# Kernel tuning notes

Hardware: AMD Instinct MI355X
Metric: run time of the kernel (lower is better)

## Reference

```python
import jax, jax.numpy as jnp
import numpy as np

INF = 1000.0
T = 1.0
NQ, NS, D, C = 4096, 8192, 512, 1024


def setup_inputs() -> dict:
    key = jax.random.key(0)
    k1, k2, k3 = jax.random.split(key, 3)
    xq = jax.random.normal(k1, (NQ, D), dtype=jnp.float32)
    xs = jax.random.normal(k2, (NS, D), dtype=jnp.float32)
    yq = jax.random.randint(k3, (NQ,), 0, C, dtype=jnp.int32)
    # supports laid out so class c occupies indices c, c+C, c+2C, ...
    ys = (jnp.arange(NS) % C).astype(jnp.int32)
    # positive index for query i: first support of class yq[i] -> index yq[i]
    pos = yq.astype(jnp.int32)
    return {"xq": xq, "yq": yq, "xs": xs, "ys": ys, "pos": pos}


def reference(xq, yq, xs, ys, pos):
    nq = xq.shape[0]
    ind = jnp.arange(nq)

    # per-class support counts (classes are 0..C-1, all present)
    counts = jax.ops.segment_sum(jnp.ones_like(ys, dtype=jnp.float32), ys,
                                 num_segments=C)  # [C]

    class_mask = yq[:, None] == ys[None, :]            # [Nq, Ns]
    idx = jnp.sum(class_mask, axis=-1) > 1             # [Nq] class has >1 support
    # drop the positive from the mask where the class has other supports
    class_mask = class_mask.at[ind, pos].set(~idx)

    # l2 logit: -||xq - xs||^2 / 2 / T
    sq = (jnp.sum(xq * xq, axis=-1)[:, None]
          + jnp.sum(xs * xs, axis=-1)[None, :]
          - 2.0 * (xq @ xs.T))                          # [Nq, Ns]
    logit = -0.5 * sq / T

    # logit[ind,pos] *= 0 then -= INF where idx  ->  0 or -INF at the positive
    logit = logit.at[ind, pos].set(jnp.where(idx, -INF, 0.0))

    # per-class masked segment sum over supports: [Nq, C]
    summed = jax.ops.segment_sum(logit.T, ys, num_segments=C).T

    # counts with the query's own class decremented by 1
    adjusted_counts = counts[None, :] - jax.nn.one_hot(yq, C, dtype=jnp.float32)
    normalized = summed / adjusted_counts               # [Nq, C]

    neg_logit = jax.nn.logsumexp(normalized, axis=1, keepdims=True)  # [Nq,1]

    mask_f = class_mask.astype(logit.dtype)
    pos_logit = (jnp.sum(logit * mask_f, axis=-1)
                 / jnp.sum(mask_f, axis=-1))[:, None]   # [Nq,1]

    return jnp.mean(neg_logit - pos_logit)
```

## Files before the change

kernel.cpp:

```cpp
#include <hip/hip_runtime.h>

#define NQ 4096
#define NS 8192
#define DD 512
#define CC 1024
#define KSUP 8
#define TM 128
#define TN 128
#define TK 64
#define KTILES (DD / TK)
#define PARTS (CC / TN)
#define NPANEL (NQ / TM)
#define CBLK (CC / 4)
#define FP_SCALE 1099511627776.0

typedef __attribute__((ext_vector_type(4))) float f32x4;

__device__ __forceinline__ unsigned int pk4_fp8(float4 v) {
    int lo = __builtin_amdgcn_cvt_pk_fp8_f32(v.x, v.y, 0, false);
    int hi = __builtin_amdgcn_cvt_pk_fp8_f32(v.z, v.w, lo, true);
    return (unsigned int)hi;
}

__device__ __forceinline__ float wave_reduce(float v) {
    #pragma unroll
    for (int d = 32; d > 0; d >>= 1) v += __shfl_xor(v, d);
    return v;
}

__global__ __launch_bounds__(256) void prep_kernel(
    const float* __restrict__ xs, const float* __restrict__ xq,
    const int* __restrict__ pos,
    unsigned char* __restrict__ Sb, float* __restrict__ SN,
    unsigned char* __restrict__ xqb, float* __restrict__ qn,
    float* __restrict__ tpl, unsigned long long* __restrict__ acc_fixed,
    unsigned int* __restrict__ panel_cnt) {
    int b = blockIdx.x, t = threadIdx.x;
    int w = t >> 6, lane = t & 63;
    if (b < CBLK) {
        if (b == 0) {
            if (t < 2) acc_fixed[t] = 0ULL;
            if (t < NPANEL) panel_cnt[t] = 0u;
        }
        int c = 4 * b + w;
        float4 s0 = {0.f, 0.f, 0.f, 0.f}, s1 = {0.f, 0.f, 0.f, 0.f};
        float nrm = 0.f;
        #pragma unroll
        for (int k = 0; k < KSUP; ++k) {
            const float4* rowp = (const float4*)(xs + (size_t)(c + k * CC) * DD);
            float4 v0 = rowp[lane];
            float4 v1 = rowp[lane + 64];
            s0.x += v0.x; s0.y += v0.y; s0.z += v0.z; s0.w += v0.w;
            s1.x += v1.x; s1.y += v1.y; s1.z += v1.z; s1.w += v1.w;
            nrm += v0.x * v0.x + v0.y * v0.y + v0.z * v0.z + v0.w * v0.w
                 + v1.x * v1.x + v1.y * v1.y + v1.z * v1.z + v1.w * v1.w;
        }
        unsigned int* dst = (unsigned int*)(Sb + (size_t)c * DD);
        dst[lane]      = pk4_fp8(s0);
        dst[lane + 64] = pk4_fp8(s1);
        nrm = wave_reduce(nrm);
        if (lane == 0) SN[c] = nrm;
    } else {
        int half = t >> 7, tt = t & 127;
        __shared__ float ws0[4], ws1[4], ws2[4];
        int i = 2 * (b - CBLK) + half;
        int j = pos[i];
        float4 q = ((const float4*)(xq + (size_t)i * DD))[tt];
        float4 s = ((const float4*)(xs + (size_t)j * DD))[tt];
        ((unsigned int*)(xqb + (size_t)i * DD))[tt] = pk4_fp8(q);
        float a  = q.x * q.x + q.y * q.y + q.z * q.z + q.w * q.w;
        float bd = q.x * s.x + q.y * s.y + q.z * s.z + q.w * s.w;
        float c2 = s.x * s.x + s.y * s.y + s.z * s.z + s.w * s.w;
        a = wave_reduce(a); bd = wave_reduce(bd); c2 = wave_reduce(c2);
        if (lane == 0) { ws0[w] = a; ws1[w] = bd; ws2[w] = c2; }
        __syncthreads();
        if (tt == 0) {
            float A  = ws0[2 * half] + ws0[2 * half + 1];
            float B  = ws1[2 * half] + ws1[2 * half + 1];
            float C2 = ws2[2 * half] + ws2[2 * half + 1];
            qn[i] = A;
            tpl[i] = -0.5f * (A + C2) + B;
        }
    }
}

__global__ __launch_bounds__(512, 2) void gemm_fused_kernel(
    const unsigned char* __restrict__ Abf,
    const unsigned char* __restrict__ Bbf,
    const float* __restrict__ SN, const float* __restrict__ qn,
    const float* __restrict__ tpl, const int* __restrict__ yq,
    float2* __restrict__ partials,
    float* __restrict__ pos_out,
    unsigned int* __restrict__ panel_cnt,
    unsigned long long* __restrict__ acc_fixed, float* __restrict__ out) {
    __shared__ __align__(16) char smem[131072];
    __shared__ unsigned int last_flag;
    __shared__ float red2[8];
    char* As = smem;
    char* Bs = smem + 65536;

    int lin = blockIdx.y * PARTS + blockIdx.x;
    int xcd = lin & 7;
    int k_in = lin >> 3;
    int bm = 4 * xcd + (k_in >> 3);
    int bn = k_in & 7;

    int t = threadIdx.x;
    int lane = t & 63, w = t >> 6;
    int wr = w & 1, wc = w >> 1;
    int r16 = lane & 15, halfk = lane >> 4;

    const int rowA0 = bm * TM;
    const int rowB0 = bn * TN;

    #pragma unroll
    for (int u = 0; u < 8; ++u) {
        int p = t + u * 512;
        int row = p >> 5, s16 = p & 31;
        int src16 = s16 ^ (row & 15);
        __builtin_amdgcn_global_load_lds(
            (const __attribute__((address_space(1))) unsigned int*)(Abf + (size_t)(rowA0 + row) * DD + src16 * 16),
            (__attribute__((address_space(3))) unsigned int*)(As + p * 16), 16, 0, 0);
    }
    #pragma unroll
    for (int u = 0; u < 8; ++u) {
        int p = t + u * 512;
        int row = p >> 5, s16 = p & 31;
        int src16 = s16 ^ (row & 15);
        __builtin_amdgcn_global_load_lds(
            (const __attribute__((address_space(1))) unsigned int*)(Bbf + (size_t)(rowB0 + row) * DD + src16 * 16),
            (__attribute__((address_space(3))) unsigned int*)(Bs + p * 16), 16, 0, 0);
    }
    asm volatile("s_waitcnt vmcnt(0)" ::: "memory");
    __builtin_amdgcn_s_barrier();
    asm volatile("" ::: "memory");

    f32x4 acc[4][2] = {};
    #pragma unroll
    for (int kt = 0; kt < KTILES; ++kt) {
        long a[4][2], bb[2][2];
        #pragma unroll
        for (int mi = 0; mi < 4; ++mi)
            #pragma unroll
            for (int kk = 0; kk < 2; ++kk) {
                int row = wr * 64 + mi * 16 + r16;
                int hk8 = kt * 8 + kk * 4 + halfk;
                a[mi][kk] = *(const long*)(As + row * 512 + ((hk8 ^ ((row & 15) << 1)) << 3));
            }
        #pragma unroll
        for (int ni = 0; ni < 2; ++ni)
            #pragma unroll
            for (int kk = 0; kk < 2; ++kk) {
                int row = wc * 32 + ni * 16 + r16;
                int hk8 = kt * 8 + kk * 4 + halfk;
                bb[ni][kk] = *(const long*)(Bs + row * 512 + ((hk8 ^ ((row & 15) << 1)) << 3));
            }
        #pragma unroll
        for (int kk = 0; kk < 2; ++kk)
            #pragma unroll
            for (int mi = 0; mi < 4; ++mi)
                #pragma unroll
                for (int ni = 0; ni < 2; ++ni)
                    acc[mi][ni] = __builtin_amdgcn_mfma_f32_16x16x32_fp8_fp8(a[mi][kk], bb[ni][kk], acc[mi][ni], 0, 0, 0);
    }

    __syncthreads();

    float* e_qn  = (float*)smem;
    float* e_tpl = e_qn + TM;
    int*   e_y   = (int*)(e_tpl + TM);
    float* e_sn  = (float*)(e_y + TM);
    float* e_max = e_sn + TN;
    float* e_sum = e_max + TM * 4;

    if (t < TM) {
        e_qn[t]  = qn[rowA0 + t];
        e_tpl[t] = tpl[rowA0 + t];
        e_y[t]   = yq[rowA0 + t];
    }
    if (t < TN) e_sn[t] = SN[rowB0 + t];
    __syncthreads();

    #pragma unroll
    for (int mi = 0; mi < 4; ++mi) {
        #pragma unroll
        for (int r = 0; r < 4; ++r) {
            int row_l = wr * 64 + mi * 16 + halfk * 4 + r;
            float base = -4.0f * e_qn[row_l];
            int yv = e_y[row_l];
            float v[2];
            #pragma unroll
            for (int ni = 0; ni < 2; ++ni) {
                int col_l = wc * 32 + ni * 16 + r16;
                float s = acc[mi][ni][r] + base - 0.5f * e_sn[col_l];
                if (rowB0 + col_l == yv) {
                    s = s - e_tpl[row_l] - 1000.0f;
                    v[ni] = s * (1.0f / 7.0f);
                    pos_out[rowA0 + row_l] = (s + 1000.0f) * (1.0f / 7.0f);
                } else {
                    v[ni] = s * 0.125f;
                }
            }
            float m = fmaxf(v[0], v[1]);
            #pragma unroll
            for (int d = 1; d < 16; d <<= 1) m = fmaxf(m, __shfl_xor(m, d));
            float sm = __expf(v[0] - m) + __expf(v[1] - m);
            #pragma unroll
            for (int d = 1; d < 16; d <<= 1) sm += __shfl_xor(sm, d);
            if (r16 == 0) {
                e_max[row_l * 4 + wc] = m;
                e_sum[row_l * 4 + wc] = sm;
            }
        }
    }
    __syncthreads();
    if (t < TM) {
        float m0 = e_max[t * 4], m1 = e_max[t * 4 + 1];
        float m2 = e_max[t * 4 + 2], m3 = e_max[t * 4 + 3];
        float g = fmaxf(fmaxf(m0, m1), fmaxf(m2, m3));
        float gs = e_sum[t * 4]     * __expf(m0 - g)
                 + e_sum[t * 4 + 1] * __expf(m1 - g)
                 + e_sum[t * 4 + 2] * __expf(m2 - g)
                 + e_sum[t * 4 + 3] * __expf(m3 - g);
        partials[(size_t)(rowA0 + t) * PARTS + bn] = make_float2(g, gs);
    }
    __syncthreads();

    if (t == 0) {
        unsigned int old = atomicAdd(&panel_cnt[bm], 1u);
        last_flag = (old == PARTS - 1) ? 1u : 0u;
    }
    __syncthreads();
    asm volatile("" ::: "memory");
    if (last_flag) {
        float loss = 0.f;
        if (t < TM) {
            int row = rowA0 + t;
            const float4* p4 = (const float4*)(partials + (size_t)row * PARTS);
            float2 pp[PARTS];
            #pragma unroll
            for (int k2 = 0; k2 < PARTS / 2; ++k2) {
                float4 v = p4[k2];
                pp[2 * k2]     = make_float2(v.x, v.y);
                pp[2 * k2 + 1] = make_float2(v.z, v.w);
            }
            float gmax = pp[0].x;
            #pragma unroll
            for (int k2 = 1; k2 < PARTS; ++k2) gmax = fmaxf(gmax, pp[k2].x);
            float gsum = 0.f;
            #pragma unroll
            for (int k2 = 0; k2 < PARTS; ++k2) gsum += pp[k2].y * __expf(pp[k2].x - gmax);
            loss = gmax + logf(gsum) - pos_out[row];
        }
        loss = wave_reduce(loss);
        if (lane == 0) red2[w] = loss;
        __syncthreads();
        if (t == 0) {
            float tot = red2[0] + red2[1] + red2[2] + red2[3]
                      + red2[4] + red2[5] + red2[6] + red2[7];
            long long fx = (long long)((double)tot * FP_SCALE);
            atomicAdd(acc_fixed, (unsigned long long)fx);
            asm volatile("s_waitcnt vmcnt(0)" ::: "memory");
            unsigned long long done = atomicAdd(acc_fixed + 1, 1ULL);
            if (done == (unsigned long long)(NPANEL - 1)) {
                unsigned long long s = atomicAdd(acc_fixed, 0ULL);
                out[0] = (float)((double)(long long)s / FP_SCALE / (double)NQ);
            }
        }
    }
}

extern "C" void kernel_launch(void* const* d_in, const int* in_sizes, int n_in,
                              void* d_out, int out_size, void* d_ws, size_t ws_size,
                              hipStream_t stream) {
    const float* xq = (const float*)d_in[0];
    const int*   yq = (const int*)d_in[1];
    const float* xs = (const float*)d_in[2];
    const int*   pos = (const int*)d_in[4];
    float* out = (float*)d_out;

    char* ws = (char*)d_ws;
    unsigned char* xqb = (unsigned char*)ws;
    unsigned char* Sb  = xqb + (size_t)NQ * DD;
    float* SN  = (float*)(Sb + (size_t)CC * DD);
    float* qn  = SN + CC;
    float* tpl = qn + NQ;
    float2* partials = (float2*)(tpl + NQ);
    float* pos_out = (float*)(partials + (size_t)NQ * PARTS);
    unsigned long long* acc_fixed = (unsigned long long*)(pos_out + NQ);
    unsigned int* panel_cnt = (unsigned int*)(acc_fixed + 2);

    hipLaunchKernelGGL(prep_kernel, dim3(CBLK + NQ / 2), dim3(256), 0, stream,
                       xs, xq, pos, Sb, SN, xqb, qn, tpl, acc_fixed, panel_cnt);
    hipLaunchKernelGGL(gemm_fused_kernel, dim3(PARTS, NQ / TM), dim3(512), 0, stream,
                       xqb, Sb, SN, qn, tpl, yq, partials, pos_out, panel_cnt, acc_fixed, out);
}
```

Baseline: 27.27 us.

## Fuse prep and GEMM into one cooperative kernel with grid sync

Merges the preprocessing kernel (fp8 class-sum supports, query fp8 packing, norms, positive logits) into the GEMM kernel, launched cooperatively with 256 blocks and a grid-wide barrier between the phases. Half the waves in each block compute class sums and the other half handle 16 queries each, with loads batched into registers for more memory-level parallelism. This removes one kernel launch and its gap. In exchange it adds a grid-sync cost and requires all 256 blocks to be co-resident, which the 131 KB of shared memory per block makes tight.

```diff
diff --git a/kernel.cpp b/kernel.cpp
--- a/kernel.cpp
+++ b/kernel.cpp
@@ -1,4 +1,7 @@
 #include <hip/hip_runtime.h>
+#include <hip/hip_cooperative_groups.h>
+
+namespace cg = cooperative_groups;
 
 #define NQ 4096
 #define NS 8192
@@ -11,7 +14,6 @@
 #define KTILES (DD / TK)
 #define PARTS (CC / TN)
 #define NPANEL (NQ / TM)
-#define CBLK (CC / 4)
 #define FP_SCALE 1099511627776.0
 
 typedef __attribute__((ext_vector_type(4))) float f32x4;
@@ -28,32 +30,62 @@
     return v;
 }
 
-__global__ __launch_bounds__(256) void prep_kernel(
-    const float* __restrict__ xs, const float* __restrict__ xq,
-    const int* __restrict__ pos,
-    unsigned char* __restrict__ Sb, float* __restrict__ SN,
-    unsigned char* __restrict__ xqb, float* __restrict__ qn,
-    float* __restrict__ tpl, unsigned long long* __restrict__ acc_fixed,
-    unsigned int* __restrict__ panel_cnt) {
-    int b = blockIdx.x, t = threadIdx.x;
-    int w = t >> 6, lane = t & 63;
-    if (b < CBLK) {
-        if (b == 0) {
-            if (t < 2) acc_fixed[t] = 0ULL;
-            if (t < NPANEL) panel_cnt[t] = 0u;
-        }
-        int c = 4 * b + w;
+__global__ __launch_bounds__(512, 2) void fused_kernel(
+    const float* __restrict__ xq, const float* __restrict__ xs,
+    const int* __restrict__ pos, const int* __restrict__ yq,
+    unsigned char* __restrict__ xqb,
+    unsigned char* __restrict__ Sb,
+    float* __restrict__ SN, float* __restrict__ qn, float* __restrict__ tpl,
+    float2* __restrict__ partials,
+    float* __restrict__ pos_out,
+    unsigned int* __restrict__ panel_cnt,
+    unsigned long long* __restrict__ acc_fixed, float* __restrict__ out)
+{
+    __shared__ __align__(16) char smem[131072];
+    __shared__ unsigned int last_flag;
+    __shared__ float red2[8];
+    char* As = smem;
+    char* Bs = smem + 65536;
+
+    int lin = blockIdx.x;
+    int xcd = lin & 7;
+    int k_in = lin >> 3;
+    int bm = 4 * xcd + (k_in >> 3);
+    int bn = k_in & 7;
+
+    int t = threadIdx.x;
+    int lane = t & 63, w = t >> 6;
+    int wr = w & 1, wc = w >> 1;
+    int r16 = lane & 15, halfk = lane >> 4;
+
+    const int rowA0 = bm * TM;
+    const int rowB0 = bn * TN;
+
+    if (lin == 0) {
+        if (t < 2)
+            __hip_atomic_store(&acc_fixed[t], 0ULL, __ATOMIC_RELAXED, __HIP_MEMORY_SCOPE_AGENT);
+        if (t < NPANEL)
+            __hip_atomic_store(&panel_cnt[t], 0u, __ATOMIC_RELAXED, __HIP_MEMORY_SCOPE_AGENT);
+    }
+
+    if (w < 4) {
+        int c = 4 * lin + w;
+        float4 v[16];
+        #pragma unroll
+        for (int k = 0; k < KSUP; ++k) {
+            const float4* rowp = (const float4*)(xs + (size_t)(c + k * CC) * DD);
+            v[2 * k]     = rowp[lane];
+            v[2 * k + 1] = rowp[lane + 64];
+        }
         float4 s0 = {0.f, 0.f, 0.f, 0.f}, s1 = {0.f, 0.f, 0.f, 0.f};
         float nrm = 0.f;
         #pragma unroll
         for (int k = 0; k < KSUP; ++k) {
-            const float4* rowp = (const float4*)(xs + (size_t)(c + k * CC) * DD);
-            float4 v0 = rowp[lane];
-            float4 v1 = rowp[lane + 64];
-            s0.x += v0.x; s0.y += v0.y; s0.z += v0.z; s0.w += v0.w;
-            s1.x += v1.x; s1.y += v1.y; s1.z += v1.z; s1.w += v1.w;
-            nrm += v0.x * v0.x + v0.y * v0.y + v0.z * v0.z + v0.w * v0.w
-                 + v1.x * v1.x + v1.y * v1.y + v1.z * v1.z + v1.w * v1.w;
+            float4 a = v[2 * k], d = v[2 * k + 1];
+            s0.x += a.x; s0.y += a.y; s0.z += a.z; s0.w += a.w;
+            s1.x += d.x; s1.y += d.y; s1.z += d.z; s1.w += d.w;
+            nrm += a.x * a.x + a.y * a.y + a.z * a.z + a.w * a.w
+                 + d.x * d.x + d.y * d.y + d.z * d.z + d.w * d.w;
         }
         unsigned int* dst = (unsigned int*)(Sb + (size_t)c * DD);
         dst[lane]      = pk4_fp8(s0);
@@ -61,57 +93,40 @@
         nrm = wave_reduce(nrm);
         if (lane == 0) SN[c] = nrm;
     } else {
-        int half = t >> 7, tt = t & 127;
-        __shared__ float ws0[4], ws1[4], ws2[4];
-        int i = 2 * (b - CBLK) + half;
-        int j = pos[i];
-        float4 q = ((const float4*)(xq + (size_t)i * DD))[tt];
-        float4 s = ((const float4*)(xs + (size_t)j * DD))[tt];
-        ((unsigned int*)(xqb + (size_t)i * DD))[tt] = pk4_fp8(q);
-        float a  = q.x * q.x + q.y * q.y + q.z * q.z + q.w * q.w;
-        float bd = q.x * s.x + q.y * s.y + q.z * s.z + q.w * s.w;
-        float c2 = s.x * s.x + s.y * s.y + s.z * s.z + s.w * s.w;
-        a = wave_reduce(a); bd = wave_reduce(bd); c2 = wave_reduce(c2);
-        if (lane == 0) { ws0[w] = a; ws1[w] = bd; ws2[w] = c2; }
-        __syncthreads();
-        if (tt == 0) {
-            float A  = ws0[2 * half] + ws0[2 * half + 1];
-            float B  = ws1[2 * half] + ws1[2 * half + 1];
-            float C2 = ws2[2 * half] + ws2[2 * half + 1];
-            qn[i] = A;
-            tpl[i] = -0.5f * (A + C2) + B;
-        }
-    }
-}
-
-__global__ __launch_bounds__(512, 2) void gemm_fused_kernel(
-    const unsigned char* __restrict__ Abf,
-    const unsigned char* __restrict__ Bbf,
-    const float* __restrict__ SN, const float* __restrict__ qn,
-    const float* __restrict__ tpl, const int* __restrict__ yq,
-    float2* __restrict__ partials,
-    float* __restrict__ pos_out,
-    unsigned int* __restrict__ panel_cnt,
-    unsigned long long* __restrict__ acc_fixed, float* __restrict__ out) {
-    __shared__ __align__(16) char smem[131072];
-    __shared__ unsigned int last_flag;
-    __shared__ float red2[8];
-    char* As = smem;
-    char* Bs = smem + 65536;
-
-    int lin = blockIdx.y * PARTS + blockIdx.x;
-    int xcd = lin & 7;
-    int k_in = lin >> 3;
-    int bm = 4 * xcd + (k_in >> 3);
-    int bn = k_in & 7;
-
-    int t = threadIdx.x;
-    int lane = t & 63, w = t >> 6;
-    int wr = w & 1, wc = w >> 1;
-    int r16 = lane & 15, halfk = lane >> 4;
-
-    const int rowA0 = bm * TM;
-    const int rowB0 = bn * TN;
+        int qbase = rowA0 + bn * 16 + (w - 4) * 4;
+        int pj[4];
+        #pragma unroll
+        for (int k = 0; k < 4; ++k) pj[k] = pos[qbase + k];
+        float4 qv[8], sv[8];
+        #pragma unroll
+        for (int k = 0; k < 4; ++k) {
+            const float4* qp = (const float4*)(xq + (size_t)(qbase + k) * DD);
+            const float4* sp = (const float4*)(xs + (size_t)pj[k] * DD);
+            qv[2 * k]     = qp[lane];
+            qv[2 * k + 1] = qp[lane + 64];
+            sv[2 * k]     = sp[lane];
+            sv[2 * k + 1] = sp[lane + 64];
+        }
+        #pragma unroll
+        for (int k = 0; k < 4; ++k) {
+            int i = qbase + k;
+            float4 qa = qv[2 * k], qd = qv[2 * k + 1];
+            float4 sa = sv[2 * k], sd = sv[2 * k + 1];
+            unsigned int* dq = (unsigned int*)(xqb + (size_t)i * DD);
+            dq[lane]      = pk4_fp8(qa);
+            dq[lane + 64] = pk4_fp8(qd);
+            float a  = qa.x * qa.x + qa.y * qa.y + qa.z * qa.z + qa.w * qa.w
+                     + qd.x * qd.x + qd.y * qd.y + qd.z * qd.z + qd.w * qd.w;
+            float bd = qa.x * sa.x + qa.y * sa.y + qa.z * sa.z + qa.w * sa.w
+                     + qd.x * sd.x + qd.y * sd.y + qd.z * sd.z + qd.w * sd.w;
+            float c2 = sa.x * sa.x + sa.y * sa.y + sa.z * sa.z + sa.w * sa.w
+                     + sd.x * sd.x + sd.y * sd.y + sd.z * sd.z + sd.w * sd.w;
+            a = wave_reduce(a); bd = wave_reduce(bd); c2 = wave_reduce(c2);
+            if (lane == 0) { qn[i] = a; tpl[i] = -0.5f * (a + c2) + bd; }
+        }
+    }
+
+    cg::this_grid().sync();
 
     #pragma unroll
     for (int u = 0; u < 8; ++u) {
@@ -119,7 +134,7 @@
         int row = p >> 5, s16 = p & 31;
         int src16 = s16 ^ (row & 15);
         __builtin_amdgcn_global_load_lds(
-            (const __attribute__((address_space(1))) unsigned int*)(Abf + (size_t)(rowA0 + row) * DD + src16 * 16),
+            (const __attribute__((address_space(1))) unsigned int*)(xqb + (size_t)(rowA0 + row) * DD + src16 * 16),
             (__attribute__((address_space(3))) unsigned int*)(As + p * 16), 16, 0, 0);
     }
     #pragma unroll
@@ -128,7 +143,7 @@
         int row = p >> 5, s16 = p & 31;
         int src16 = s16 ^ (row & 15);
         __builtin_amdgcn_global_load_lds(
-            (const __attribute__((address_space(1))) unsigned int*)(Bbf + (size_t)(rowB0 + row) * DD + src16 * 16),
+            (const __attribute__((address_space(1))) unsigned int*)(Sb + (size_t)(rowB0 + row) * DD + src16 * 16),
             (__attribute__((address_space(3))) unsigned int*)(Bs + p * 16), 16, 0, 0);
     }
     asm volatile("s_waitcnt vmcnt(0)" ::: "memory");
@@ -290,8 +305,11 @@
     unsigned long long* acc_fixed = (unsigned long long*)(pos_out + NQ);
     unsigned int* panel_cnt = (unsigned int*)(acc_fixed + 2);
 
-    hipLaunchKernelGGL(prep_kernel, dim3(CBLK + NQ / 2), dim3(256), 0, stream,
-                       xs, xq, pos, Sb, SN, xqb, qn, tpl, acc_fixed, panel_cnt);
-    hipLaunchKernelGGL(gemm_fused_kernel, dim3(PARTS, NQ / TM), dim3(512), 0, stream,
-                       xqb, Sb, SN, qn, tpl, yq, partials, pos_out, panel_cnt, acc_fixed, out);
+    void* args[] = {
+        (void*)&xq, (void*)&xs, (void*)&pos, (void*)&yq,
+        (void*)&xqb, (void*)&Sb, (void*)&SN, (void*)&qn, (void*)&tpl,
+        (void*)&partials, (void*)&pos_out, (void*)&panel_cnt,
+        (void*)&acc_fixed, (void*)&out
+    };
+    hipLaunchCooperativeKernel(fused_kernel, dim3(256), dim3(512), args, 0, stream);
 }
```

Result: slower. 66.68 us (+144.6%).

## Split K-dimension load into two halves and overlap second half with MFMA

Applied to the files above, without the earlier changes.

Global-to-LDS loads for the A and B tiles are issued in two K-halves (first 256 bytes, then second 256 bytes per row) into separate LDS regions with a per-half swizzle. The kernel waits only for the first half (vmcnt(8)) before starting MFMAs, then waits for the rest at kt==4. This hides part of the load latency behind compute, at the cost of an extra barrier and changed LDS addressing.

```diff
diff --git a/kernel.cpp b/kernel.cpp
--- a/kernel.cpp
+++ b/kernel.cpp
@@ -114,46 +114,69 @@
     const int rowB0 = bn * TN;
 
     #pragma unroll
-    for (int u = 0; u < 8; ++u) {
-        int p = t + u * 512;
-        int row = p >> 5, s16 = p & 31;
-        int src16 = s16 ^ (row & 15);
+    for (int u = 0; u < 4; ++u) {
+        int q = t + u * 512;
+        int row = q >> 4, src = (q & 15) ^ (row & 15);
         __builtin_amdgcn_global_load_lds(
-            (const __attribute__((address_space(1))) unsigned int*)(Abf + (size_t)(rowA0 + row) * DD + src16 * 16),
-            (__attribute__((address_space(3))) unsigned int*)(As + p * 16), 16, 0, 0);
-    }
-    #pragma unroll
-    for (int u = 0; u < 8; ++u) {
-        int p = t + u * 512;
-        int row = p >> 5, s16 = p & 31;
-        int src16 = s16 ^ (row & 15);
+            (const __attribute__((address_space(1))) unsigned int*)(Abf + (size_t)(rowA0 + row) * DD + src * 16),
+            (__attribute__((address_space(3))) unsigned int*)(As + q * 16), 16, 0, 0);
+    }
+    #pragma unroll
+    for (int u = 0; u < 4; ++u) {
+        int q = t + u * 512;
+        int row = q >> 4, src = (q & 15) ^ (row & 15);
         __builtin_amdgcn_global_load_lds(
-            (const __attribute__((address_space(1))) unsigned int*)(Bbf + (size_t)(rowB0 + row) * DD + src16 * 16),
-            (__attribute__((address_space(3))) unsigned int*)(Bs + p * 16), 16, 0, 0);
-    }
-    asm volatile("s_waitcnt vmcnt(0)" ::: "memory");
+            (const __attribute__((address_space(1))) unsigned int*)(Bbf + (size_t)(rowB0 + row) * DD + src * 16),
+            (__attribute__((address_space(3))) unsigned int*)(Bs + q * 16), 16, 0, 0);
+    }
+    #pragma unroll
+    for (int u = 0; u < 4; ++u) {
+        int q = t + u * 512;
+        int row = q >> 4, src = (q & 15) ^ (row & 15);
+        __builtin_amdgcn_global_load_lds(
+            (const __attribute__((address_space(1))) unsigned int*)(Abf + (size_t)(rowA0 + row) * DD + 256 + src * 16),
+            (__attribute__((address_space(3))) unsigned int*)(As + 32768 + q * 16), 16, 0, 0);
+    }
+    #pragma unroll
+    for (int u = 0; u < 4; ++u) {
+        int q = t + u * 512;
+        int row = q >> 4, src = (q & 15) ^ (row & 15);
+        __builtin_amdgcn_global_load_lds(
+            (const __attribute__((address_space(1))) unsigned int*)(Bbf + (size_t)(rowB0 + row) * DD + 256 + src * 16),
+            (__attribute__((address_space(3))) unsigned int*)(Bs + 32768 + q * 16), 16, 0, 0);
+    }
+    asm volatile("s_waitcnt vmcnt(8)" ::: "memory");
     __builtin_amdgcn_s_barrier();
-    asm volatile("" ::: "memory");
+    __builtin_amdgcn_sched_barrier(0);
 
     f32x4 acc[4][2] = {};
     #pragma unroll
     for (int kt = 0; kt < KTILES; ++kt) {
+        if (kt == 4) {
+            __builtin_amdgcn_sched_barrier(0);
+            asm volatile("s_waitcnt vmcnt(0)" ::: "memory");
+            __builtin_amdgcn_s_barrier();
+            __builtin_amdgcn_sched_barrier(0);
+        }
+        const char* Ah = As + (kt >> 2) * 32768;
+        const char* Bh = Bs + (kt >> 2) * 32768;
+        int ktl = kt & 3;
         long a[4][2], bb[2][2];
         #pragma unroll
         for (int mi = 0; mi < 4; ++mi)
             #pragma unroll
             for (int kk = 0; kk < 2; ++kk) {
                 int row = wr * 64 + mi * 16 + r16;
-                int hk8 = kt * 8 + kk * 4 + halfk;
-                a[mi][kk] = *(const long*)(As + row * 512 + ((hk8 ^ ((row & 15) << 1)) << 3));
+                int hh = ktl * 8 + kk * 4 + halfk;
+                a[mi][kk] = *(const long*)(Ah + row * 256 + ((hh ^ ((row & 15) << 1)) << 3));
             }
         #pragma unroll
         for (int ni = 0; ni < 2; ++ni)
             #pragma unroll
             for (int kk = 0; kk < 2; ++kk) {
                 int row = wc * 32 + ni * 16 + r16;
-                int hk8 = kt * 8 + kk * 4 + halfk;
-                bb[ni][kk] = *(const long*)(Bs + row * 512 + ((hk8 ^ ((row & 15) << 1)) << 3));
+                int hh = ktl * 8 + kk * 4 + halfk;
+                bb[ni][kk] = *(const long*)(Bh + row * 256 + ((hh ^ ((row & 15) << 1)) << 3));
             }
         #pragma unroll
         for (int kk = 0; kk < 2; ++kk)
```

Result: no change. 27.37 us (+0.4%).
